# Kernel tuning notes

Measured on AMD Instinct MI355X. Metric: run time of the kernel, lower is better.

The kernel has to match this reference:

```python
import jax, jax.numpy as jnp
import numpy as np

B, P, D, V, T = 2048, 20, 64, 100000, 33  # batch, pool_size, embedding_dim, vocab per table, num tables
F_IN = 35 * D  # 2 raw features repeated + 33 embeddings, concatenated


def setup_inputs() -> dict:
    key = jax.random.key(0)
    ks = jax.random.split(key, 7)
    def lin(k, fan_in, shape):
        return (jax.random.uniform(k, shape, jnp.float32, -1.0, 1.0) / np.sqrt(fan_in)).astype(jnp.float32)
    return {
        "x_raw": jax.random.normal(ks[0], (B, P, 2), jnp.float32),
        "x_idx": jax.random.randint(ks[1], (B, P, T), 0, V, jnp.int32),
        "emb": jax.random.normal(ks[2], (T, V, D), jnp.float32),
        "W1": lin(ks[3], F_IN, (F_IN, 512)), "b1": jnp.zeros((512,), jnp.float32),
        "W2": lin(ks[4], 512, (512, 256)), "b2": jnp.zeros((256,), jnp.float32),
        "W3": lin(ks[5], 256, (256, 1)), "b3": jnp.zeros((1,), jnp.float32),
    }


def reference(x_raw, x_idx, emb, W1, b1, W2, b2, W3, b3):
    # 33 per-table gathers, vectorized: emb[t, x_idx[..., t]] -> [B, P, T, D]
    e = emb[jnp.arange(T)[None, None, :], x_idx]
    # raw features repeated along embedding dim -> [B, P, 2, D]
    raw = jnp.broadcast_to(x_raw[..., None], x_raw.shape + (D,))
    feat = jnp.concatenate([raw, e], axis=2).reshape(x_raw.shape[0], x_raw.shape[1], F_IN)
    # dropout p=0.0 (eval) -> identity
    h = jax.nn.relu(feat @ W1 + b1)
    h = jax.nn.relu(h @ W2 + b2)
    logit = h @ W3 + b3  # [B, P, 1]
    return jax.nn.softmax(logit, axis=1)
```

## Files before the change

### kernel.cpp

```cpp
#include <hip/hip_runtime.h>
#include <hip/hip_bf16.h>
#include <stdint.h>

#define B_   2048
#define P_   20
#define D_   64
#define V_   100000
#define T_   33
#define FIN  2240
#define KE   2112
#define M_   (B_*P_)
#define H1_  512
#define H2_  256
#define NKT  33

using bf16 = __hip_bfloat16;
typedef __bf16 bf16x8 __attribute__((ext_vector_type(8)));
typedef float  f32x4  __attribute__((ext_vector_type(4)));

__device__ __forceinline__ void gload16(const void* g, void* l) {
    __builtin_amdgcn_global_load_lds(
        (const __attribute__((address_space(1))) uint32_t*)g,
        (__attribute__((address_space(3))) uint32_t*)l, 16, 0, 0);
}
__device__ __forceinline__ void gload4(const void* g, void* l) {
    __builtin_amdgcn_global_load_lds(
        (const __attribute__((address_space(1))) uint32_t*)g,
        (__attribute__((address_space(3))) uint32_t*)l, 4, 0, 0);
}

__global__ __launch_bounds__(256) void colsum_k(
    const float* __restrict__ W1, float* __restrict__ S01)
{
    int g = blockIdx.x * 256 + threadIdx.x;
    int s = g >> 9, n = g & 511;
    const float* p = W1 + (size_t)(s * 64) * H1_ + n;
    float acc = 0.f;
    #pragma unroll 8
    for (int k = 0; k < 64; ++k) acc += p[(size_t)k * H1_];
    S01[s * H1_ + n] = acc;
}

__global__ __launch_bounds__(256) void w1t_k(
    const float* __restrict__ W1, bf16* __restrict__ W1t)
{
    int idx = blockIdx.x * 256 + threadIdx.x;
    int n = idx / KE;
    int k = idx - n * KE;
    W1t[idx] = __float2bfloat16(W1[(size_t)(k + 128) * H1_ + n]);
}

__global__ __launch_bounds__(256) void transpose_bf16_k(
    const float* __restrict__ W, bf16* __restrict__ Wt, int K, int N)
{
    int idx = blockIdx.x * 256 + threadIdx.x;
    if (idx >= N * K) return;
    int n = idx / K;
    int k = idx - n * K;
    Wt[idx] = __float2bfloat16(W[(size_t)k * N + n]);
}

__global__ __launch_bounds__(512, 2) void fused_gemm1_k(
    const float* __restrict__ x_raw, const int* __restrict__ x_idx,
    const float* __restrict__ emb, const bf16* __restrict__ W1t,
    const float* __restrict__ b1, const float* __restrict__ S01,
    bf16* __restrict__ h1)
{
    extern __shared__ char smem[];
    char* Als  = smem;
    char* Bls  = smem + 81920;
    char* ring = smem + 81920 + 65536;

    const int tid = threadIdx.x;
    const int w  = tid >> 6, l = tid & 63;
    const int wr = w >> 2, wc = w & 3;
    const int fr = l & 15, fq = l >> 4;
    const int m0 = blockIdx.x * 160;

    const int arow_sub = l >> 4;
    const int acol     = l & 15;
    const int brow_sub = l >> 2;
    const int bcol     = l & 3;

    f32x4 acc[5][8] = {};

    auto issue_idx = [&](int t, int slot) {
        if (l < 20)
            gload4((const char*)x_idx + ((size_t)(m0 + w * 20 + l) * T_ + t) * 4,
                   ring + slot * 640 + w * 80);
    };
    auto issue_A = [&](int t, int buf, const int (&iv)[5]) {
        char* dst = Als + buf * 40960 + (w * 20) * 256;
        #pragma unroll
        for (int p = 0; p < 5; ++p) {
            int row = w * 20 + p * 4 + arow_sub;
            const char* src = (const char*)(emb + ((size_t)t * V_ + (size_t)iv[p]) * D_)
                              + ((acol * 16) ^ ((row & 7) << 4));
            gload16(src, dst + p * 1024);
        }
    };
    auto issue_B = [&](int t, int h) {
        char* dst = Bls + h * 32768 + w * 4096;
        #pragma unroll
        for (int i = 0; i < 4; ++i) {
            int row = w * 64 + i * 16 + brow_sub;
            const char* src = (const char*)W1t + ((size_t)row * KE + t * 64 + h * 32) * 2
                              + ((bcol * 16) ^ ((row & 3) << 4));
            gload16(src, dst + i * 1024);
        }
    };
    auto read_iv = [&](int slot, int (&iv)[5]) {
        const int* ivp = (const int*)(ring + slot * 640 + w * 80);
        #pragma unroll
        for (int p = 0; p < 5; ++p) iv[p] = ivp[p * 4 + arow_sub];
    };
    auto mfma_half = [&](int abuf, int kk) {
        const char* Ab = Als + abuf * 40960;
        bf16x8 af[5];
        #pragma unroll
        for (int i = 0; i < 5; ++i) {
            int r  = wr * 80 + i * 16 + fr;
            int xr = (r & 7) << 4;
            float4 a0 = *(const float4*)(Ab + r * 256 + ((kk * 128 + fq * 32) ^ xr));
            float4 a1 = *(const float4*)(Ab + r * 256 + ((kk * 128 + fq * 32 + 16) ^ xr));
            bf16x8 t;
            t[0] = (__bf16)a0.x; t[1] = (__bf16)a0.y;
            t[2] = (__bf16)a0.z; t[3] = (__bf16)a0.w;
            t[4] = (__bf16)a1.x; t[5] = (__bf16)a1.y;
            t[6] = (__bf16)a1.z; t[7] = (__bf16)a1.w;
            af[i] = t;
        }
        const char* Bb = Bls + kk * 32768;
        #pragma unroll
        for (int j = 0; j < 8; ++j) {
            int n = wc * 128 + j * 16 + fr;
            bf16x8 bg = *(const bf16x8*)(Bb + n * 64 + ((fq * 16) ^ ((n & 3) << 4)));
            #pragma unroll
            for (int i = 0; i < 5; ++i)
                acc[i][j] = __builtin_amdgcn_mfma_f32_16x16x32_bf16(
                    af[i], bg, acc[i][j], 0, 0, 0);
        }
    };

    int iv[5];
    issue_idx(0, 0);
    asm volatile("s_waitcnt vmcnt(0)" ::: "memory");
    read_iv(0, iv);
    issue_A(0, 0, iv);
    issue_idx(1, 1);
    issue_B(0, 0);
    issue_B(0, 1);

    for (int kt = 0; kt < NKT; ++kt) {
        int tA = (kt + 1 < NKT) ? kt + 1 : NKT - 1;
        int t2 = (kt + 2 < NKT) ? kt + 2 : NKT - 1;

        asm volatile("s_waitcnt vmcnt(8)" ::: "memory");
        read_iv((kt + 1) & 1, iv);
        issue_A(tA, (kt + 1) & 1, iv);
        issue_idx(t2, kt & 1);
        asm volatile("s_waitcnt vmcnt(10)" ::: "memory");
        __builtin_amdgcn_s_barrier();
        __builtin_amdgcn_sched_barrier(0);

        __builtin_amdgcn_s_setprio(1);
        mfma_half(kt & 1, 0);
        __builtin_amdgcn_s_setprio(0);
        asm volatile("s_waitcnt lgkmcnt(0)" ::: "memory");
        __builtin_amdgcn_s_barrier();

        issue_B(tA, 0);
        asm volatile("s_waitcnt vmcnt(10)" ::: "memory");
        __builtin_amdgcn_s_barrier();
        __builtin_amdgcn_sched_barrier(0);

        __builtin_amdgcn_s_setprio(1);
        mfma_half(kt & 1, 1);
        __builtin_amdgcn_s_setprio(0);
        asm volatile("s_waitcnt lgkmcnt(0)" ::: "memory");
        __builtin_amdgcn_s_barrier();

        issue_B(tA, 1);
    }
    asm volatile("s_waitcnt vmcnt(0)" ::: "memory");

    const float* S0 = S01;
    const float* S1 = S01 + H1_;
    #pragma unroll
    for (int i = 0; i < 5; ++i) {
        int rbase = wr * 80 + i * 16 + fq * 4;
        float x0[4], x1[4];
        #pragma unroll
        for (int r2 = 0; r2 < 4; ++r2) {
            int m = m0 + rbase + r2;
            x0[r2] = x_raw[2 * m];
            x1[r2] = x_raw[2 * m + 1];
        }
        #pragma unroll
        for (int j = 0; j < 8; ++j) {
            int n = wc * 128 + j * 16 + fr;
            float bb = b1[n], s0 = S0[n], s1 = S1[n];
            #pragma unroll
            for (int r2 = 0; r2 < 4; ++r2) {
                float v = acc[i][j][r2] + bb + x0[r2] * s0 + x1[r2] * s1;
                h1[(size_t)(m0 + rbase + r2) * H1_ + n] =
                    __float2bfloat16(fmaxf(v, 0.0f));
            }
        }
    }
}

__global__ __launch_bounds__(512) void gemm2_head_k(
    const bf16* __restrict__ h1, const bf16* __restrict__ W2t,
    const float* __restrict__ b2, const float* __restrict__ W3,
    const float* __restrict__ b3, float* __restrict__ out)
{
    __shared__ char  As[20480];
    __shared__ char  Bs[32768];
    __shared__ float w3s[H2_];
    __shared__ float b2s[H2_];
    __shared__ float logq[4][160];
    __shared__ float logits[160];

    const int tid = threadIdx.x;
    const int w = tid >> 6, l = tid & 63;
    const int wr = w >> 2, wc = w & 3;
    const int fr = l & 15, fq = l >> 4;
    const int m0 = blockIdx.x * 160;
    const int r8 = l >> 3, c8 = l & 7;

    if (tid < H2_) { w3s[tid] = W3[tid]; b2s[tid] = b2[tid]; }

    f32x4 acc[5][4] = {};

    for (int kt = 0; kt < 8; ++kt) {
        for (int s = w; s < 20; s += 8) {
            int row = s * 8 + r8;
            const char* src = (const char*)(h1 + (size_t)(m0 + row) * H1_ + kt * 64)
                              + ((16 * c8) ^ ((row & 7) << 4));
            gload16(src, As + s * 1024);
        }
        #pragma unroll
        for (int q = 0; q < 4; ++q) {
            int s = q * 8 + w;
            int row = s * 8 + r8;
            const char* src = (const char*)(W2t + (size_t)row * H1_ + kt * 64)
                              + ((16 * c8) ^ ((row & 7) << 4));
            gload16(src, Bs + s * 1024);
        }
        __syncthreads();

        #pragma unroll
        for (int kk = 0; kk < 2; ++kk) {
            bf16x8 af[5];
            #pragma unroll
            for (int i = 0; i < 5; ++i) {
                int r = wr * 80 + i * 16 + fr;
                int byte = (r * 128 + kk * 64 + fq * 16) ^ ((r & 7) << 4);
                af[i] = *(const bf16x8*)(As + byte);
            }
            #pragma unroll
            for (int j = 0; j < 4; ++j) {
                int n = wc * 64 + j * 16 + fr;
                int byte = (n * 128 + kk * 64 + fq * 16) ^ ((n & 7) << 4);
                bf16x8 bg = *(const bf16x8*)(Bs + byte);
                #pragma unroll
                for (int i = 0; i < 5; ++i)
                    acc[i][j] = __builtin_amdgcn_mfma_f32_16x16x32_bf16(
                        af[i], bg, acc[i][j], 0, 0, 0);
            }
        }
        __syncthreads();
    }

    #pragma unroll
    for (int i = 0; i < 5; ++i) {
        #pragma unroll
        for (int r2 = 0; r2 < 4; ++r2) {
            float s = 0.f;
            #pragma unroll
            for (int j = 0; j < 4; ++j) {
                int col = wc * 64 + j * 16 + fr;
                float v = fmaxf(acc[i][j][r2] + b2s[col], 0.f);
                s += v * w3s[col];
            }
            #pragma unroll
            for (int off = 1; off < 16; off <<= 1) s += __shfl_xor(s, off);
            if (fr == 0)
                logq[wc][wr * 80 + i * 16 + fq * 4 + r2] = s;
        }
    }
    __syncthreads();
    if (tid < 160)
        logits[tid] = logq[0][tid] + logq[1][tid] + logq[2][tid] + logq[3][tid] + b3[0];
    __syncthreads();
    if (tid < 160) {
        int bb = (tid / 20) * 20;
        float mx = -1e30f;
        #pragma unroll
        for (int p = 0; p < 20; ++p) mx = fmaxf(mx, logits[bb + p]);
        float sum = 0.f;
        #pragma unroll
        for (int p = 0; p < 20; ++p) sum += expf(logits[bb + p] - mx);
        out[m0 + tid] = expf(logits[tid] - mx) / sum;
    }
}

extern "C" void kernel_launch(void* const* d_in, const int* in_sizes, int n_in,
                              void* d_out, int out_size, void* d_ws, size_t ws_size,
                              hipStream_t stream)
{
    const float* x_raw = (const float*)d_in[0];
    const int*   x_idx = (const int*)  d_in[1];
    const float* emb   = (const float*)d_in[2];
    const float* W1    = (const float*)d_in[3];
    const float* b1    = (const float*)d_in[4];
    const float* W2    = (const float*)d_in[5];
    const float* b2    = (const float*)d_in[6];
    const float* W3    = (const float*)d_in[7];
    const float* b3    = (const float*)d_in[8];

    char* ws = (char*)d_ws;
    size_t off = 0;
    bf16*  W1t = (bf16*) (ws + off); off += (size_t)H1_ * KE * 2;
    bf16*  W2t = (bf16*) (ws + off); off += (size_t)H2_ * H1_ * 2;
    float* S01 = (float*)(ws + off); off += (size_t)2 * H1_ * 4;
    bf16*  h1  = (bf16*) (ws + off); off += (size_t)M_ * H1_ * 2;

    colsum_k<<<4, 256, 0, stream>>>(W1, S01);
    w1t_k<<<(H1_ * KE) / 256, 256, 0, stream>>>(W1, W1t);
    transpose_bf16_k<<<(H2_ * H1_ + 255) / 256, 256, 0, stream>>>(W2, W2t, H1_, H2_);

    hipFuncSetAttribute((const void*)fused_gemm1_k,
                        hipFuncAttributeMaxDynamicSharedMemorySize, 148736);
    fused_gemm1_k<<<256, 512, 148736, stream>>>(x_raw, x_idx, emb, W1t, b1, S01, h1);

    gemm2_head_k<<<256, 512, 0, stream>>>(h1, W2t, b2, W3, b3, (float*)d_out);
}
```

Before: 187.2 us.

## Fuse second GEMM and softmax head into first GEMM kernel via LDS

Merges the layer-2 GEMM, ReLU, W3 projection and per-batch softmax into the layer-1 kernel. The bf16 h1 activations are kept in registers and staged through LDS in 64-column chunks, while W2t chunks are double-buffered from global memory. This removes the h1 round trip through global memory (about 42 MB written and read back) and one kernel launch. In exchange it raises register pressure in an already heavy kernel and serialises the epilogue GEMM behind barriers, since only one wave column writes each A chunk.

```diff
diff --git a/kernel.cpp b/kernel.cpp
--- a/kernel.cpp
+++ b/kernel.cpp
@@ -28,6 +28,23 @@
         (const __attribute__((address_space(1))) uint32_t*)g,
         (__attribute__((address_space(3))) uint32_t*)l, 4, 0, 0);
 }
+__device__ __forceinline__ unsigned short b16bits(float f) {
+    return __builtin_bit_cast(unsigned short, __float2bfloat16(f));
+}
+
+#define OFF_BLS   81920
+#define OFF_RING  147456
+#define OFF_ACH   0
+#define OFF_BCH   40960
+#define OFF_W3S   106496
+#define OFF_B2S   107520
+#define OFF_B1S   108544
+#define OFF_S0S   110592
+#define OFF_S1S   112640
+#define OFF_XRS   114688
+#define OFF_LOGQ  115968
+#define OFF_LOG   118528
+#define LDS_BYTES 148736
 
 __global__ __launch_bounds__(256) void colsum_k(
     const float* __restrict__ W1, float* __restrict__ S01)
@@ -60,16 +77,18 @@
     Wt[idx] = __float2bfloat16(W[(size_t)k * N + n]);
 }
 
-__global__ __launch_bounds__(512, 2) void fused_gemm1_k(
+__global__ __launch_bounds__(512, 2) void mega_k(
     const float* __restrict__ x_raw, const int* __restrict__ x_idx,
     const float* __restrict__ emb, const bf16* __restrict__ W1t,
     const float* __restrict__ b1, const float* __restrict__ S01,
-    bf16* __restrict__ h1)
+    const bf16* __restrict__ W2t, const float* __restrict__ b2,
+    const float* __restrict__ W3, const float* __restrict__ b3,
+    float* __restrict__ out)
 {
     extern __shared__ char smem[];
     char* Als  = smem;
-    char* Bls  = smem + 81920;
-    char* ring = smem + 81920 + 65536;
+    char* Bls  = smem + OFF_BLS;
+    char* ring = smem + OFF_RING;
 
     const int tid = threadIdx.x;
     const int w  = tid >> 6, l = tid & 63;
@@ -184,115 +203,163 @@
     }
     asm volatile("s_waitcnt vmcnt(0)" ::: "memory");
 
-    const float* S0 = S01;
-    const float* S1 = S01 + H1_;
+    auto epi_issue = [&](int kc2) {
+        char* dst = smem + OFF_BCH + (kc2 & 1) * 32768 + w * 4096;
+        #pragma unroll
+        for (int q = 0; q < 4; ++q) {
+            int row = w * 32 + q * 8 + (l >> 3);
+            const char* src = (const char*)W2t + (size_t)row * 1024 + kc2 * 128
+                              + (((l & 7) ^ (row & 7)) * 16);
+            gload16(src, dst + q * 1024);
+        }
+    };
+
+    if (tid < 512) {
+        ((float*)(smem + OFF_B1S))[tid] = b1[tid];
+        ((float*)(smem + OFF_S0S))[tid] = S01[tid];
+        ((float*)(smem + OFF_S1S))[tid] = S01[512 + tid];
+    }
+    if (tid < 256) {
+        ((float*)(smem + OFF_W3S))[tid] = W3[tid];
+        ((float*)(smem + OFF_B2S))[tid] = b2[tid];
+    }
+    if (tid < 160)
+        ((float2*)(smem + OFF_XRS))[tid] = ((const float2*)x_raw)[m0 + tid];
+
+    epi_issue(0);
+    epi_issue(1);
+    __syncthreads();
+
+    uint32_t h1b[5][8][2];
     #pragma unroll
     for (int i = 0; i < 5; ++i) {
         int rbase = wr * 80 + i * 16 + fq * 4;
-        float x0[4], x1[4];
-        #pragma unroll
-        for (int r2 = 0; r2 < 4; ++r2) {
-            int m = m0 + rbase + r2;
-            x0[r2] = x_raw[2 * m];
-            x1[r2] = x_raw[2 * m + 1];
-        }
+        float4 xa = *(const float4*)(smem + OFF_XRS + rbase * 8);
+        float4 xb = *(const float4*)(smem + OFF_XRS + rbase * 8 + 16);
+        float x0[4] = {xa.x, xa.z, xb.x, xb.z};
+        float x1[4] = {xa.y, xa.w, xb.y, xb.w};
         #pragma unroll
         for (int j = 0; j < 8; ++j) {
             int n = wc * 128 + j * 16 + fr;
-            float bb = b1[n], s0 = S0[n], s1 = S1[n];
-            #pragma unroll
-            for (int r2 = 0; r2 < 4; ++r2) {
-                float v = acc[i][j][r2] + bb + x0[r2] * s0 + x1[r2] * s1;
-                h1[(size_t)(m0 + rbase + r2) * H1_ + n] =
-                    __float2bfloat16(fmaxf(v, 0.0f));
+            float bb = *(const float*)(smem + OFF_B1S + n * 4);
+            float s0 = *(const float*)(smem + OFF_S0S + n * 4);
+            float s1 = *(const float*)(smem + OFF_S1S + n * 4);
+            #pragma unroll
+            for (int q = 0; q < 2; ++q) {
+                float v0 = fmaxf(acc[i][j][2*q]   + bb + x0[2*q]*s0   + x1[2*q]*s1,   0.f);
+                float v1 = fmaxf(acc[i][j][2*q+1] + bb + x0[2*q+1]*s0 + x1[2*q+1]*s1, 0.f);
+                h1b[i][j][q] = (uint32_t)b16bits(v0) | ((uint32_t)b16bits(v1) << 16);
             }
         }
     }
-}
-
-__global__ __launch_bounds__(512) void gemm2_head_k(
-    const bf16* __restrict__ h1, const bf16* __restrict__ W2t,
-    const float* __restrict__ b2, const float* __restrict__ W3,
-    const float* __restrict__ b3, float* __restrict__ out)
-{
-    __shared__ char  As[20480];
-    __shared__ char  Bs[32768];
-    __shared__ float w3s[H2_];
-    __shared__ float b2s[H2_];
-    __shared__ float logq[4][160];
-    __shared__ float logits[160];
-
-    const int tid = threadIdx.x;
-    const int w = tid >> 6, l = tid & 63;
-    const int wr = w >> 2, wc = w & 3;
-    const int fr = l & 15, fq = l >> 4;
-    const int m0 = blockIdx.x * 160;
-    const int r8 = l >> 3, c8 = l & 7;
-
-    if (tid < H2_) { w3s[tid] = W3[tid]; b2s[tid] = b2[tid]; }
-
-    f32x4 acc[5][4] = {};
-
-    for (int kt = 0; kt < 8; ++kt) {
-        for (int s = w; s < 20; s += 8) {
-            int row = s * 8 + r8;
-            const char* src = (const char*)(h1 + (size_t)(m0 + row) * H1_ + kt * 64)
-                              + ((16 * c8) ^ ((row & 7) << 4));
-            gload16(src, As + s * 1024);
-        }
-        #pragma unroll
-        for (int q = 0; q < 4; ++q) {
-            int s = q * 8 + w;
-            int row = s * 8 + r8;
-            const char* src = (const char*)(W2t + (size_t)row * H1_ + kt * 64)
-                              + ((16 * c8) ^ ((row & 7) << 4));
-            gload16(src, Bs + s * 1024);
-        }
-        __syncthreads();
-
+
+    f32x4 acc2[5][4] = {};
+
+    auto epi_write = [&](int kc) {
+        if (wc == (kc >> 1)) {
+            char* Ach = smem + OFF_ACH + (kc & 1) * 20480;
+            #pragma unroll
+            for (int i = 0; i < 5; ++i) {
+                #pragma unroll
+                for (int jj = 0; jj < 4; ++jj) {
+                    int j = (kc & 1) * 4 + jj;
+                    #pragma unroll
+                    for (int q = 0; q < 2; ++q) {
+                        uint32_t p2 = h1b[i][j][q];
+                        int rw0 = wr * 80 + i * 16 + fq * 4 + 2 * q;
+                        int cb  = (jj * 16 + fr) * 2;
+                        *(uint16_t*)(Ach + ((rw0 * 128 + cb) ^ ((rw0 & 7) << 4)))
+                            = (uint16_t)p2;
+                        int rw1 = rw0 + 1;
+                        *(uint16_t*)(Ach + ((rw1 * 128 + cb) ^ ((rw1 & 7) << 4)))
+                            = (uint16_t)(p2 >> 16);
+                    }
+                }
+            }
+        }
+    };
+    auto epi_mfma = [&](int kc) {
+        const char* Ach = smem + OFF_ACH + (kc & 1) * 20480;
+        const char* Bch = smem + OFF_BCH + (kc & 1) * 32768;
         #pragma unroll
         for (int kk = 0; kk < 2; ++kk) {
             bf16x8 af[5];
             #pragma unroll
             for (int i = 0; i < 5; ++i) {
                 int r = wr * 80 + i * 16 + fr;
-                int byte = (r * 128 + kk * 64 + fq * 16) ^ ((r & 7) << 4);
-                af[i] = *(const bf16x8*)(As + byte);
+                af[i] = *(const bf16x8*)(Ach + ((r * 128 + kk * 64 + fq * 16)
+                                                ^ ((r & 7) << 4)));
             }
             #pragma unroll
-            for (int j = 0; j < 4; ++j) {
-                int n = wc * 64 + j * 16 + fr;
-                int byte = (n * 128 + kk * 64 + fq * 16) ^ ((n & 7) << 4);
-                bf16x8 bg = *(const bf16x8*)(Bs + byte);
+            for (int j2 = 0; j2 < 4; ++j2) {
+                int n2 = wc * 64 + j2 * 16 + fr;
+                bf16x8 bg = *(const bf16x8*)(Bch + ((n2 * 128 + kk * 64 + fq * 16)
+                                                    ^ ((n2 & 7) << 4)));
                 #pragma unroll
                 for (int i = 0; i < 5; ++i)
-                    acc[i][j] = __builtin_amdgcn_mfma_f32_16x16x32_bf16(
-                        af[i], bg, acc[i][j], 0, 0, 0);
+                    acc2[i][j2] = __builtin_amdgcn_mfma_f32_16x16x32_bf16(
+                        af[i], bg, acc2[i][j2], 0, 0, 0);
             }
         }
-        __syncthreads();
-    }
-
+    };
+
+    epi_write(0);
+    asm volatile("s_waitcnt lgkmcnt(0)" ::: "memory");
+    __builtin_amdgcn_s_barrier();
+    epi_mfma(0);
+    asm volatile("s_waitcnt lgkmcnt(0)" ::: "memory");
+    __builtin_amdgcn_s_barrier();
+    epi_issue(2);
+    epi_write(1);
+    asm volatile("s_waitcnt lgkmcnt(0)" ::: "memory");
+    __builtin_amdgcn_s_barrier();
+    epi_mfma(1);
+    asm volatile("s_waitcnt lgkmcnt(0)" ::: "memory");
+    __builtin_amdgcn_s_barrier();
+    epi_issue(3);
+    #pragma unroll
+    for (int kc = 2; kc <= 6; ++kc) {
+        epi_write(kc);
+        asm volatile("s_waitcnt lgkmcnt(0)" ::: "memory");
+        asm volatile("s_waitcnt vmcnt(4)" ::: "memory");
+        __builtin_amdgcn_s_barrier();
+        epi_mfma(kc);
+        asm volatile("s_waitcnt lgkmcnt(0)" ::: "memory");
+        __builtin_amdgcn_s_barrier();
+        if (kc + 2 <= 7) epi_issue(kc + 2);
+    }
+    epi_write(7);
+    asm volatile("s_waitcnt lgkmcnt(0)" ::: "memory");
+    asm volatile("s_waitcnt vmcnt(0)" ::: "memory");
+    __builtin_amdgcn_s_barrier();
+    epi_mfma(7);
+    asm volatile("s_waitcnt lgkmcnt(0)" ::: "memory");
+    __builtin_amdgcn_s_barrier();
+
+    float* logq   = (float*)(smem + OFF_LOGQ);
+    float* logits = (float*)(smem + OFF_LOG);
     #pragma unroll
     for (int i = 0; i < 5; ++i) {
         #pragma unroll
         for (int r2 = 0; r2 < 4; ++r2) {
             float s = 0.f;
             #pragma unroll
-            for (int j = 0; j < 4; ++j) {
-                int col = wc * 64 + j * 16 + fr;
-                float v = fmaxf(acc[i][j][r2] + b2s[col], 0.f);
-                s += v * w3s[col];
+            for (int j2 = 0; j2 < 4; ++j2) {
+                int n2 = wc * 64 + j2 * 16 + fr;
+                float v = fmaxf(acc2[i][j2][r2]
+                                + *(const float*)(smem + OFF_B2S + n2 * 4), 0.f);
+                s += v * *(const float*)(smem + OFF_W3S + n2 * 4);
             }
             #pragma unroll
             for (int off = 1; off < 16; off <<= 1) s += __shfl_xor(s, off);
             if (fr == 0)
-                logq[wc][wr * 80 + i * 16 + fq * 4 + r2] = s;
+                logq[wc * 160 + wr * 80 + i * 16 + fq * 4 + r2] = s;
         }
     }
     __syncthreads();
     if (tid < 160)
-        logits[tid] = logq[0][tid] + logq[1][tid] + logq[2][tid] + logq[3][tid] + b3[0];
+        logits[tid] = logq[tid] + logq[160 + tid] + logq[320 + tid]
+                    + logq[480 + tid] + b3[0];
     __syncthreads();
     if (tid < 160) {
         int bb = (tid / 20) * 20;
@@ -325,15 +392,13 @@
     bf16*  W1t = (bf16*) (ws + off); off += (size_t)H1_ * KE * 2;
     bf16*  W2t = (bf16*) (ws + off); off += (size_t)H2_ * H1_ * 2;
     float* S01 = (float*)(ws + off); off += (size_t)2 * H1_ * 4;
-    bf16*  h1  = (bf16*) (ws + off); off += (size_t)M_ * H1_ * 2;
 
     colsum_k<<<4, 256, 0, stream>>>(W1, S01);
     w1t_k<<<(H1_ * KE) / 256, 256, 0, stream>>>(W1, W1t);
     transpose_bf16_k<<<(H2_ * H1_ + 255) / 256, 256, 0, stream>>>(W2, W2t, H1_, H2_);
 
-    hipFuncSetAttribute((const void*)fused_gemm1_k,
-                        hipFuncAttributeMaxDynamicSharedMemorySize, 148736);
-    fused_gemm1_k<<<256, 512, 148736, stream>>>(x_raw, x_idx, emb, W1t, b1, S01, h1);
-
-    gemm2_head_k<<<256, 512, 0, stream>>>(h1, W2t, b2, W3, b3, (float*)d_out);
-}
+    hipFuncSetAttribute((const void*)mega_k,
+                        hipFuncAttributeMaxDynamicSharedMemorySize, LDS_BYTES);
+    mega_k<<<256, 512, LDS_BYTES, stream>>>(x_raw, x_idx, emb, W1t, b1, S01,
+                                            W2t, b2, W3, b3, (float*)d_out);
+}
```

New measurement: 349.4 us. 1.87x slower.

## Retile gemm1 to 320x256 tiles with register-staged bf16 embedding gathers

Applied to the files above, without the earlier changes.

Changes the fused embedding-gather GEMM1 tile from 160 rows by 512 columns to 320 rows by 256 columns, with a block-to-tile mapping that pairs the two N halves, so each W1 column slice is reused across more rows. Embedding rows are now loaded into registers, converted to bf16 once, and written to swizzled LDS instead of being copied to LDS as fp32 by direct-to-LDS loads. This halves the A-tile LDS footprint for the larger tile and removes the per-MFMA fp32-to-bf16 conversion. In exchange each embedding row is gathered twice (once per N half), it uses more registers and VALU work to stage loads, and the hand-tuned waitcnt accounting has to stay correct.

```diff
diff --git a/kernel.cpp b/kernel.cpp
--- a/kernel.cpp
+++ b/kernel.cpp
@@ -28,6 +28,9 @@
         (const __attribute__((address_space(1))) uint32_t*)g,
         (__attribute__((address_space(3))) uint32_t*)l, 4, 0, 0);
 }
+__device__ __forceinline__ unsigned short b16bits(float f) {
+    return __builtin_bit_cast(unsigned short, __float2bfloat16(f));
+}
 
 __global__ __launch_bounds__(256) void colsum_k(
     const float* __restrict__ W1, float* __restrict__ S01)
@@ -69,68 +72,77 @@
     extern __shared__ char smem[];
     char* Als  = smem;
     char* Bls  = smem + 81920;
-    char* ring = smem + 81920 + 65536;
+    char* ring = smem + 81920 + 32768;
 
     const int tid = threadIdx.x;
     const int w  = tid >> 6, l = tid & 63;
-    const int wr = w >> 2, wc = w & 3;
+    const int wr = w >> 1, wc = w & 1;
     const int fr = l & 15, fq = l >> 4;
-    const int m0 = blockIdx.x * 160;
-
-    const int arow_sub = l >> 4;
-    const int acol     = l & 15;
-    const int brow_sub = l >> 2;
-    const int bcol     = l & 3;
-
-    f32x4 acc[5][8] = {};
-
-    auto issue_idx = [&](int t, int slot) {
-        if (l < 20)
-            gload4((const char*)x_idx + ((size_t)(m0 + w * 20 + l) * T_ + t) * 4,
-                   ring + slot * 640 + w * 80);
-    };
-    auto issue_A = [&](int t, int buf, const int (&iv)[5]) {
-        char* dst = Als + buf * 40960 + (w * 20) * 256;
+
+    const int bid = blockIdx.x;
+    const int mt  = (bid & 7) | ((bid >> 4) << 3);
+    const int nt  = (bid >> 3) & 1;
+    const int m0  = mt * 320;
+    const int n0  = nt * 256;
+
+    const int arsub = l >> 4;
+    const int acol  = l & 15;
+    const int brsub = l >> 2;
+    const int bcol  = l & 3;
+
+    f32x4  acc[5][8] = {};
+    float4 aA[5], aB[5];
+    int    ivA[5], ivB[5];
+
+    auto issue_idx = [&](int t) {
+        if (l < 40)
+            gload4((const char*)x_idx + ((size_t)(m0 + w * 40 + l) * T_ + t) * 4,
+                   ring + (t & 1) * 1280 + w * 160);
+    };
+    auto read_iv = [&](int t, int b, int (&iv)[5]) {
+        const int* ivp = (const int*)(ring + (t & 1) * 1280 + w * 160);
+        #pragma unroll
+        for (int p = 0; p < 5; ++p) iv[p] = ivp[b * 20 + p * 4 + arsub];
+    };
+    auto issue_aregs = [&](int t, const int (&iv)[5], float4 (&ar)[5]) {
+        #pragma unroll
+        for (int p = 0; p < 5; ++p)
+            ar[p] = *reinterpret_cast<const float4*>(
+                emb + ((size_t)t * V_ + (size_t)iv[p]) * D_ + acol * 4);
+    };
+    auto write_A = [&](int buf, int b, const float4 (&ar)[5]) {
+        char* base = Als + buf * 40960;
         #pragma unroll
         for (int p = 0; p < 5; ++p) {
-            int row = w * 20 + p * 4 + arow_sub;
-            const char* src = (const char*)(emb + ((size_t)t * V_ + (size_t)iv[p]) * D_)
-                              + ((acol * 16) ^ ((row & 7) << 4));
-            gload16(src, dst + p * 1024);
+            int row = w * 40 + b * 20 + p * 4 + arsub;
+            ushort4 o;
+            o.x = b16bits(ar[p].x); o.y = b16bits(ar[p].y);
+            o.z = b16bits(ar[p].z); o.w = b16bits(ar[p].w);
+            int byte = (row * 128 + acol * 8) ^ ((row & 7) << 4);
+            *reinterpret_cast<ushort4*>(base + byte) = o;
         }
     };
     auto issue_B = [&](int t, int h) {
-        char* dst = Bls + h * 32768 + w * 4096;
-        #pragma unroll
-        for (int i = 0; i < 4; ++i) {
-            int row = w * 64 + i * 16 + brow_sub;
-            const char* src = (const char*)W1t + ((size_t)row * KE + t * 64 + h * 32) * 2
-                              + ((bcol * 16) ^ ((row & 3) << 4));
+        char* dst = Bls + h * 16384 + w * 2048;
+        #pragma unroll
+        for (int i = 0; i < 2; ++i) {
+            int row = w * 32 + i * 16 + brsub;
+            const char* src = (const char*)W1t
+                + ((size_t)(n0 + row) * KE + t * 64 + h * 32) * 2
+                + ((bcol * 16) ^ ((row & 3) << 4));
             gload16(src, dst + i * 1024);
         }
-    };
-    auto read_iv = [&](int slot, int (&iv)[5]) {
-        const int* ivp = (const int*)(ring + slot * 640 + w * 80);
-        #pragma unroll
-        for (int p = 0; p < 5; ++p) iv[p] = ivp[p * 4 + arow_sub];
     };
     auto mfma_half = [&](int abuf, int kk) {
         const char* Ab = Als + abuf * 40960;
         bf16x8 af[5];
         #pragma unroll
         for (int i = 0; i < 5; ++i) {
-            int r  = wr * 80 + i * 16 + fr;
-            int xr = (r & 7) << 4;
-            float4 a0 = *(const float4*)(Ab + r * 256 + ((kk * 128 + fq * 32) ^ xr));
-            float4 a1 = *(const float4*)(Ab + r * 256 + ((kk * 128 + fq * 32 + 16) ^ xr));
-            bf16x8 t;
-            t[0] = (__bf16)a0.x; t[1] = (__bf16)a0.y;
-            t[2] = (__bf16)a0.z; t[3] = (__bf16)a0.w;
-            t[4] = (__bf16)a1.x; t[5] = (__bf16)a1.y;
-            t[6] = (__bf16)a1.z; t[7] = (__bf16)a1.w;
-            af[i] = t;
-        }
-        const char* Bb = Bls + kk * 32768;
+            int r = wr * 80 + i * 16 + fr;
+            af[i] = *(const bf16x8*)(Ab + ((r * 128 + kk * 64 + fq * 16)
+                                           ^ ((r & 7) << 4)));
+        }
+        const char* Bb = Bls + kk * 16384;
         #pragma unroll
         for (int j = 0; j < 8; ++j) {
             int n = wc * 128 + j * 16 + fr;
@@ -142,24 +154,30 @@
         }
     };
 
-    int iv[5];
-    issue_idx(0, 0);
+    issue_idx(0);
     asm volatile("s_waitcnt vmcnt(0)" ::: "memory");
-    read_iv(0, iv);
-    issue_A(0, 0, iv);
-    issue_idx(1, 1);
+    read_iv(0, 0, ivA);
+    read_iv(0, 1, ivB);
+    issue_aregs(0, ivA, aA);
+    issue_aregs(0, ivB, aB);
+    asm volatile("s_waitcnt vmcnt(0)" ::: "memory");
+    write_A(0, 0, aA);
+    write_A(0, 1, aB);
+    issue_idx(1);
     issue_B(0, 0);
     issue_B(0, 1);
+    asm volatile("s_waitcnt vmcnt(4)" ::: "memory");
+    read_iv(1, 0, ivA);
+    read_iv(1, 1, ivB);
 
     for (int kt = 0; kt < NKT; ++kt) {
         int tA = (kt + 1 < NKT) ? kt + 1 : NKT - 1;
         int t2 = (kt + 2 < NKT) ? kt + 2 : NKT - 1;
 
+        issue_aregs(tA, ivA, aA);
+        issue_idx(t2);
         asm volatile("s_waitcnt vmcnt(8)" ::: "memory");
-        read_iv((kt + 1) & 1, iv);
-        issue_A(tA, (kt + 1) & 1, iv);
-        issue_idx(t2, kt & 1);
-        asm volatile("s_waitcnt vmcnt(10)" ::: "memory");
+        asm volatile("s_waitcnt lgkmcnt(0)" ::: "memory");
         __builtin_amdgcn_s_barrier();
         __builtin_amdgcn_sched_barrier(0);
 
@@ -170,7 +188,8 @@
         __builtin_amdgcn_s_barrier();
 
         issue_B(tA, 0);
-        asm volatile("s_waitcnt vmcnt(10)" ::: "memory");
+        issue_aregs(tA, ivB, aB);
+        asm volatile("s_waitcnt vmcnt(13)" ::: "memory");
         __builtin_amdgcn_s_barrier();
         __builtin_amdgcn_sched_barrier(0);
 
@@ -180,7 +199,11 @@
         asm volatile("s_waitcnt lgkmcnt(0)" ::: "memory");
         __builtin_amdgcn_s_barrier();
 
+        write_A(kt & 1 ^ 1, 0, aA);
         issue_B(tA, 1);
+        write_A(kt & 1 ^ 1, 1, aB);
+        read_iv(t2, 0, ivA);
+        read_iv(t2, 1, ivB);
     }
     asm volatile("s_waitcnt vmcnt(0)" ::: "memory");
 
@@ -198,7 +221,7 @@
         }
         #pragma unroll
         for (int j = 0; j < 8; ++j) {
-            int n = wc * 128 + j * 16 + fr;
+            int n = n0 + wc * 128 + j * 16 + fr;
             float bb = b1[n], s0 = S0[n], s1 = S1[n];
             #pragma unroll
             for (int r2 = 0; r2 < 4; ++r2) {
@@ -332,8 +355,8 @@
     transpose_bf16_k<<<(H2_ * H1_ + 255) / 256, 256, 0, stream>>>(W2, W2t, H1_, H2_);
 
     hipFuncSetAttribute((const void*)fused_gemm1_k,
-                        hipFuncAttributeMaxDynamicSharedMemorySize, 148736);
-    fused_gemm1_k<<<256, 512, 148736, stream>>>(x_raw, x_idx, emb, W1t, b1, S01, h1);
+                        hipFuncAttributeMaxDynamicSharedMemorySize, 117248);
+    fused_gemm1_k<<<256, 512, 117248, stream>>>(x_raw, x_idx, emb, W1t, b1, S01, h1);
 
     gemm2_head_k<<<256, 512, 0, stream>>>(h1, W2t, b2, W3, b3, (float*)d_out);
 }
```

Result: slower. 394.5 us (+110.7%).

## Retile fused gather-GEMM1 to 320x256 tiles with half-K A staging

Applied to the files above, without the earlier changes.

Changes the block tile of the fused embedding-gather GEMM1 from 160 rows by all 512 columns to 320 rows by 256 columns, so each gathered embedding row is fetched by two blocks, one per N-half. In exchange each W1 tile is reused across twice as many rows. The A stage now holds one K-half in each buffer instead of double-buffering whole K-tiles, and the index prefetch and vmcnt waits are reordered to match. Shared memory use drops, which may let more blocks fit per CU. The cost is more redundant gather traffic from the embedding tables and less load/compute overlap for A.

```diff
diff --git a/kernel.cpp b/kernel.cpp
--- a/kernel.cpp
+++ b/kernel.cpp
@@ -69,60 +69,67 @@
     extern __shared__ char smem[];
     char* Als  = smem;
     char* Bls  = smem + 81920;
-    char* ring = smem + 81920 + 65536;
+    char* ring = smem + 81920 + 32768;
 
     const int tid = threadIdx.x;
     const int w  = tid >> 6, l = tid & 63;
-    const int wr = w >> 2, wc = w & 3;
+    const int wr = w >> 1, wc = w & 1;
     const int fr = l & 15, fq = l >> 4;
-    const int m0 = blockIdx.x * 160;
-
-    const int arow_sub = l >> 4;
-    const int acol     = l & 15;
-    const int brow_sub = l >> 2;
-    const int bcol     = l & 3;
+
+    const int bid = blockIdx.x;
+    const int mt  = (bid & 7) | ((bid >> 4) << 3);
+    const int nt  = (bid >> 3) & 1;
+    const int m0  = mt * 320;
+    const int n0  = nt * 256;
+
+    const int ar8 = l >> 3;
+    const int ac8 = l & 7;
+    const int br4 = l >> 2;
+    const int bc4 = l & 3;
 
     f32x4 acc[5][8] = {};
-
-    auto issue_idx = [&](int t, int slot) {
-        if (l < 20)
-            gload4((const char*)x_idx + ((size_t)(m0 + w * 20 + l) * T_ + t) * 4,
-                   ring + slot * 640 + w * 80);
-    };
-    auto issue_A = [&](int t, int buf, const int (&iv)[5]) {
-        char* dst = Als + buf * 40960 + (w * 20) * 256;
+    int iv[5];
+
+    auto issue_idx = [&](int t) {
+        if (l < 40)
+            gload4((const char*)x_idx + ((size_t)(m0 + w * 40 + l) * T_ + t) * 4,
+                   ring + (t & 1) * 1280 + w * 160);
+    };
+    auto read_iv = [&](int t) {
+        const int* ivp = (const int*)(ring + (t & 1) * 1280 + w * 160);
+        #pragma unroll
+        for (int p = 0; p < 5; ++p) iv[p] = ivp[p * 8 + ar8];
+    };
+    auto issue_A = [&](int t, int h) {
+        char* dst = Als + h * 40960 + w * 5120;
         #pragma unroll
         for (int p = 0; p < 5; ++p) {
-            int row = w * 20 + p * 4 + arow_sub;
+            int row = w * 40 + p * 8 + ar8;
             const char* src = (const char*)(emb + ((size_t)t * V_ + (size_t)iv[p]) * D_)
-                              + ((acol * 16) ^ ((row & 7) << 4));
+                              + h * 128 + ((ac8 * 16) ^ ((row & 7) << 4));
             gload16(src, dst + p * 1024);
         }
     };
     auto issue_B = [&](int t, int h) {
-        char* dst = Bls + h * 32768 + w * 4096;
-        #pragma unroll
-        for (int i = 0; i < 4; ++i) {
-            int row = w * 64 + i * 16 + brow_sub;
-            const char* src = (const char*)W1t + ((size_t)row * KE + t * 64 + h * 32) * 2
-                              + ((bcol * 16) ^ ((row & 3) << 4));
+        char* dst = Bls + h * 16384 + w * 2048;
+        #pragma unroll
+        for (int i = 0; i < 2; ++i) {
+            int row = w * 32 + i * 16 + br4;
+            const char* src = (const char*)W1t
+                + ((size_t)(n0 + row) * KE + t * 64 + h * 32) * 2
+                + ((bc4 * 16) ^ ((row & 3) << 4));
             gload16(src, dst + i * 1024);
         }
     };
-    auto read_iv = [&](int slot, int (&iv)[5]) {
-        const int* ivp = (const int*)(ring + slot * 640 + w * 80);
-        #pragma unroll
-        for (int p = 0; p < 5; ++p) iv[p] = ivp[p * 4 + arow_sub];
-    };
-    auto mfma_half = [&](int abuf, int kk) {
-        const char* Ab = Als + abuf * 40960;
+    auto mfma_half = [&](int h) {
+        const char* Ab = Als + h * 40960;
         bf16x8 af[5];
         #pragma unroll
         for (int i = 0; i < 5; ++i) {
             int r  = wr * 80 + i * 16 + fr;
             int xr = (r & 7) << 4;
-            float4 a0 = *(const float4*)(Ab + r * 256 + ((kk * 128 + fq * 32) ^ xr));
-            float4 a1 = *(const float4*)(Ab + r * 256 + ((kk * 128 + fq * 32 + 16) ^ xr));
+            float4 a0 = *(const float4*)(Ab + r * 128 + ((fq * 32) ^ xr));
+            float4 a1 = *(const float4*)(Ab + r * 128 + ((fq * 32 + 16) ^ xr));
             bf16x8 t;
             t[0] = (__bf16)a0.x; t[1] = (__bf16)a0.y;
             t[2] = (__bf16)a0.z; t[3] = (__bf16)a0.w;
@@ -130,7 +137,7 @@
             t[6] = (__bf16)a1.z; t[7] = (__bf16)a1.w;
             af[i] = t;
         }
-        const char* Bb = Bls + kk * 32768;
+        const char* Bb = Bls + h * 16384;
         #pragma unroll
         for (int j = 0; j < 8; ++j) {
             int n = wc * 128 + j * 16 + fr;
@@ -142,44 +149,44 @@
         }
     };
 
-    int iv[5];
-    issue_idx(0, 0);
+    issue_idx(0);
     asm volatile("s_waitcnt vmcnt(0)" ::: "memory");
-    read_iv(0, iv);
-    issue_A(0, 0, iv);
-    issue_idx(1, 1);
+    read_iv(0);
+    issue_A(0, 0);
     issue_B(0, 0);
+    issue_idx(1);
+    issue_A(0, 1);
     issue_B(0, 1);
 
     for (int kt = 0; kt < NKT; ++kt) {
         int tA = (kt + 1 < NKT) ? kt + 1 : NKT - 1;
         int t2 = (kt + 2 < NKT) ? kt + 2 : NKT - 1;
 
-        asm volatile("s_waitcnt vmcnt(8)" ::: "memory");
-        read_iv((kt + 1) & 1, iv);
-        issue_A(tA, (kt + 1) & 1, iv);
-        issue_idx(t2, kt & 1);
-        asm volatile("s_waitcnt vmcnt(10)" ::: "memory");
+        asm volatile("s_waitcnt vmcnt(7)" ::: "memory");
+        read_iv(tA);
         __builtin_amdgcn_s_barrier();
         __builtin_amdgcn_sched_barrier(0);
 
         __builtin_amdgcn_s_setprio(1);
-        mfma_half(kt & 1, 0);
+        mfma_half(0);
         __builtin_amdgcn_s_setprio(0);
         asm volatile("s_waitcnt lgkmcnt(0)" ::: "memory");
         __builtin_amdgcn_s_barrier();
 
+        issue_A(tA, 0);
         issue_B(tA, 0);
-        asm volatile("s_waitcnt vmcnt(10)" ::: "memory");
+        issue_idx(t2);
+        asm volatile("s_waitcnt vmcnt(8)" ::: "memory");
         __builtin_amdgcn_s_barrier();
         __builtin_amdgcn_sched_barrier(0);
 
         __builtin_amdgcn_s_setprio(1);
-        mfma_half(kt & 1, 1);
+        mfma_half(1);
         __builtin_amdgcn_s_setprio(0);
         asm volatile("s_waitcnt lgkmcnt(0)" ::: "memory");
         __builtin_amdgcn_s_barrier();
 
+        issue_A(tA, 1);
         issue_B(tA, 1);
     }
     asm volatile("s_waitcnt vmcnt(0)" ::: "memory");
@@ -198,7 +205,7 @@
         }
         #pragma unroll
         for (int j = 0; j < 8; ++j) {
-            int n = wc * 128 + j * 16 + fr;
+            int n = n0 + wc * 128 + j * 16 + fr;
             float bb = b1[n], s0 = S0[n], s1 = S1[n];
             #pragma unroll
             for (int r2 = 0; r2 < 4; ++r2) {
@@ -332,8 +339,8 @@
     transpose_bf16_k<<<(H2_ * H1_ + 255) / 256, 256, 0, stream>>>(W2, W2t, H1_, H2_);
 
     hipFuncSetAttribute((const void*)fused_gemm1_k,
-                        hipFuncAttributeMaxDynamicSharedMemorySize, 148736);
-    fused_gemm1_k<<<256, 512, 148736, stream>>>(x_raw, x_idx, emb, W1t, b1, S01, h1);
+                        hipFuncAttributeMaxDynamicSharedMemorySize, 117248);
+    fused_gemm1_k<<<256, 512, 117248, stream>>>(x_raw, x_idx, emb, W1t, b1, S01, h1);
 
     gemm2_head_k<<<256, 512, 0, stream>>>(h1, W2t, b2, W3, b3, (float*)d_out);
 }
```

Result: slower. 218.0 us (+16.4%).
